# Optimization experiments

Measured on AMD Instinct MI355X. Metric: run time of the kernel, lower is better.

## Reference

```python
import jax, jax.numpy as jnp
import numpy as np
from jax import lax

K = 35
PAD = K // 2  # 17

def _maxpool_same(x):
    # x: [B, H, W]; torch MaxPool2d pads with -inf, stride 1, same spatial size
    return lax.reduce_window(
        x, -jnp.inf, lax.max,
        window_dimensions=(1, K, K),
        window_strides=(1, 1, 1),
        padding=[(0, 0), (PAD, PAD), (PAD, PAD)],
    )

def setup_inputs() -> dict:
    key = jax.random.key(0)
    k1, k2 = jax.random.split(key)
    shape = (16, 3, 512, 512)
    restored = jax.random.uniform(k1, shape, dtype=jnp.float32)
    target = jax.random.uniform(k2, shape, dtype=jnp.float32)
    return {"restored": restored, "target": target}

def reference(restored, target):
    r = _maxpool_same(jnp.min(restored, axis=1))  # channel-min then 35x35 max
    t = _maxpool_same(jnp.min(target, axis=1))
    out = jnp.mean(jnp.abs(r - t))
    return jax.nn.sigmoid(out)
```

## Files before the change

### kernel.cpp

```cpp
#include <hip/hip_runtime.h>
#include <math.h>

#define WID 512
#define HEI 512
#define NB  16
#define HW  ((size_t)HEI * WID)
#define NEG_INF (-INFINITY)

typedef float f4 __attribute__((ext_vector_type(4)));

__global__ __launch_bounds__(256) void hmax_kernel(
    const float* __restrict__ rin, const float* __restrict__ tin,
    float* __restrict__ ws, float* __restrict__ acc)
{
    __shared__ float sm[2][552];
    const int tid = threadIdx.x;
    const int row = tid >> 7;
    const int t   = tid & 127;
    const int h   = blockIdx.x * 2 + row;
    const int z   = blockIdx.y;
    const int b   = z & 15;
    const float* __restrict__ in = (z < NB) ? rin : tin;

    if (blockIdx.x == 0 && blockIdx.y == 0 && tid < 2) acc[tid] = 0.0f;

    if (tid < 80) {
        int r2 = tid / 40, j = tid % 40;
        sm[r2][(j < 20) ? j : (j + 512)] = NEG_INF;
    }

    const float* __restrict__ p = in + (size_t)b * 3 * HW + (size_t)h * WID;
    f4 a0 = __builtin_nontemporal_load((const f4*)p + t);
    f4 a1 = __builtin_nontemporal_load((const f4*)(p + HW) + t);
    f4 a2 = __builtin_nontemporal_load((const f4*)(p + 2 * HW) + t);
    f4 v;
    v.x = fminf(fminf(a0.x, a1.x), a2.x);
    v.y = fminf(fminf(a0.y, a1.y), a2.y);
    v.z = fminf(fminf(a0.z, a1.z), a2.z);
    v.w = fminf(fminf(a0.w, a1.w), a2.w);
    *(f4*)&sm[row][20 + 4 * t] = v;
    __syncthreads();

    const f4* __restrict__ smr = (const f4*)sm[row];
    f4 vv[11];
    #pragma unroll
    for (int i = 0; i < 11; ++i) vv[i] = smr[t + i];
    float q[10];
    #pragma unroll
    for (int i = 1; i <= 9; ++i)
        q[i] = fmaxf(fmaxf(vv[i].x, vv[i].y), fmaxf(vv[i].z, vv[i].w));
    float Q28 = fmaxf(fmaxf(fmaxf(q[2], q[3]), fmaxf(q[4], q[5])),
                      fmaxf(fmaxf(q[6], q[7]), q[8]));
    float Q18 = fmaxf(Q28, q[1]);
    float Q29 = fmaxf(Q28, q[9]);
    float s01 = fmaxf(vv[9].x, vv[9].y);
    float s23 = fmaxf(vv[1].z, vv[1].w);
    f4 o;
    o.x = fmaxf(fmaxf(Q18, vv[0].w), s01);
    o.y = fmaxf(Q18, fmaxf(s01, vv[9].z));
    o.z = fmaxf(fmaxf(Q29, vv[1].y), s23);
    o.w = fmaxf(Q29, fmaxf(s23, vv[10].x));
    *((f4*)(ws + (size_t)z * HW + (size_t)h * WID) + t) = o;
}

__global__ __launch_bounds__(256) void vmax_kernel(
    const float* __restrict__ ws, float* __restrict__ acc,
    float* __restrict__ out)
{
    __shared__ float sm[98][64];
    __shared__ float red[4];
    const int tid = threadIdx.x;
    const int col = tid & 63;
    const int ty  = tid >> 6;
    const int w0  = blockIdx.x * 64;
    const int h0  = blockIdx.y * 64;
    const int b   = blockIdx.z;

    float rtv[16];
    float tsum = 0.0f;

    #pragma unroll
    for (int tensor = 0; tensor < 2; ++tensor) {
        const float* __restrict__ pb = ws + (size_t)(tensor * NB + b) * HW;
        #pragma unroll
        for (int i0 = 0; i0 < 1568; i0 += 256) {
            int i = i0 + tid;
            if (i < 1568) {
                int r = i >> 4, c4 = i & 15;
                int hh = h0 - 17 + r;
                f4 v = {NEG_INF, NEG_INF, NEG_INF, NEG_INF};
                if (hh >= 0 && hh < HEI)
                    v = ((const f4*)pb)[hh * 128 + (w0 >> 2) + c4];
                *(f4*)&sm[r][c4 * 4] = v;
            }
        }
        __syncthreads();

        float vc[50];
        #pragma unroll
        for (int i = 0; i < 50; ++i) vc[i] = sm[ty * 16 + i][col];
        float q[12];
        #pragma unroll
        for (int i = 0; i < 12; ++i)
            q[i] = fmaxf(fmaxf(vc[4*i], vc[4*i+1]), fmaxf(vc[4*i+2], vc[4*i+3]));
        #pragma unroll
        for (int m = 0; m < 4; ++m) {
            float Qc = fmaxf(fmaxf(fmaxf(q[m+1], q[m+2]), fmaxf(q[m+3], q[m+4])),
                             fmaxf(fmaxf(q[m+5], q[m+6]), q[m+7]));
            float A  = fmaxf(Qc, q[m+8]);
            float o0 = fmaxf(fmaxf(Qc, q[m]),
                             fmaxf(fmaxf(vc[4*m+32], vc[4*m+33]), vc[4*m+34]));
            float o1 = fmaxf(A, fmaxf(fmaxf(vc[4*m+1], vc[4*m+2]), vc[4*m+3]));
            float o2 = fmaxf(A, fmaxf(fmaxf(vc[4*m+2], vc[4*m+3]), vc[4*m+36]));
            float o3 = fmaxf(A, fmaxf(fmaxf(vc[4*m+3], vc[4*m+36]), vc[4*m+37]));
            if (tensor == 0) {
                rtv[4*m] = o0; rtv[4*m+1] = o1; rtv[4*m+2] = o2; rtv[4*m+3] = o3;
            } else {
                tsum += fabsf(rtv[4*m]   - o0) + fabsf(rtv[4*m+1] - o1)
                      + fabsf(rtv[4*m+2] - o2) + fabsf(rtv[4*m+3] - o3);
            }
        }
        __syncthreads();
    }

    #pragma unroll
    for (int off = 32; off > 0; off >>= 1)
        tsum += __shfl_down(tsum, off, 64);
    if ((tid & 63) == 0) red[ty] = tsum;
    __syncthreads();
    if (tid == 0) {
        float blocksum = red[0] + red[1] + red[2] + red[3];
        atomicAdd(acc, blocksum);
        __threadfence();
        unsigned tk = atomicAdd((unsigned*)(acc + 1), 1u);
        if (tk == 1023u) {
            float s = atomicAdd(acc, 0.0f);
            out[0] = 1.0f / (1.0f + expf(-s / 4194304.0f));
        }
    }
}

extern "C" void kernel_launch(void* const* d_in, const int* in_sizes, int n_in,
                              void* d_out, int out_size, void* d_ws, size_t ws_size,
                              hipStream_t stream) {
    const float* rin = (const float*)d_in[0];
    const float* tin = (const float*)d_in[1];
    float* out = (float*)d_out;

    float* wsf = (float*)d_ws;
    float* acc = wsf + (size_t)2 * NB * HW;

    dim3 gA(HEI / 2, 2 * NB);
    hipLaunchKernelGGL(hmax_kernel, gA, dim3(256), 0, stream, rin, tin, wsf, acc);

    dim3 gB(WID / 64, HEI / 64, NB);
    hipLaunchKernelGGL(vmax_kernel, gB, dim3(256), 0, stream, wsf, acc, out);
}
```

Baseline: 154.0 us.

## Fuse channel-min, horizontal and vertical max pooling into one tiled kernel

Replaces the two-kernel pipeline with a single kernel. Each block loads a halo tile of the raw inputs, takes the channel minimum, runs the horizontal 35-wide max in shared memory, then the vertical max and the reduction. This removes the full-size intermediate write and read through global memory and one kernel launch. In exchange, each block recomputes channel-min and horizontal max over halo rows and columns (98x104 tile for a 64x64 output), re-reads overlapping input, and adds a memset launch to clear the accumulator.

```diff
diff --git a/kernel.cpp b/kernel.cpp
--- a/kernel.cpp
+++ b/kernel.cpp
@@ -9,46 +9,17 @@
 
 typedef float f4 __attribute__((ext_vector_type(4)));
 
-__global__ __launch_bounds__(256) void hmax_kernel(
-    const float* __restrict__ rin, const float* __restrict__ tin,
-    float* __restrict__ ws, float* __restrict__ acc)
-{
-    __shared__ float sm[2][552];
-    const int tid = threadIdx.x;
-    const int row = tid >> 7;
-    const int t   = tid & 127;
-    const int h   = blockIdx.x * 2 + row;
-    const int z   = blockIdx.y;
-    const int b   = z & 15;
-    const float* __restrict__ in = (z < NB) ? rin : tin;
+__device__ __forceinline__ float qmax4(f4 v) {
+    return fmaxf(fmaxf(v.x, v.y), fmaxf(v.z, v.w));
+}
 
-    if (blockIdx.x == 0 && blockIdx.y == 0 && tid < 2) acc[tid] = 0.0f;
-
-    if (tid < 80) {
-        int r2 = tid / 40, j = tid % 40;
-        sm[r2][(j < 20) ? j : (j + 512)] = NEG_INF;
-    }
-
-    const float* __restrict__ p = in + (size_t)b * 3 * HW + (size_t)h * WID;
-    f4 a0 = __builtin_nontemporal_load((const f4*)p + t);
-    f4 a1 = __builtin_nontemporal_load((const f4*)(p + HW) + t);
-    f4 a2 = __builtin_nontemporal_load((const f4*)(p + 2 * HW) + t);
-    f4 v;
-    v.x = fminf(fminf(a0.x, a1.x), a2.x);
-    v.y = fminf(fminf(a0.y, a1.y), a2.y);
-    v.z = fminf(fminf(a0.z, a1.z), a2.z);
-    v.w = fminf(fminf(a0.w, a1.w), a2.w);
-    *(f4*)&sm[row][20 + 4 * t] = v;
-    __syncthreads();
-
-    const f4* __restrict__ smr = (const f4*)sm[row];
+__device__ __forceinline__ f4 hwin35(const f4* __restrict__ rp, int c4) {
     f4 vv[11];
     #pragma unroll
-    for (int i = 0; i < 11; ++i) vv[i] = smr[t + i];
+    for (int i = 0; i < 11; ++i) vv[i] = rp[c4 + i];
     float q[10];
     #pragma unroll
-    for (int i = 1; i <= 9; ++i)
-        q[i] = fmaxf(fmaxf(vv[i].x, vv[i].y), fmaxf(vv[i].z, vv[i].w));
+    for (int i = 1; i <= 9; ++i) q[i] = qmax4(vv[i]);
     float Q28 = fmaxf(fmaxf(fmaxf(q[2], q[3]), fmaxf(q[4], q[5])),
                       fmaxf(fmaxf(q[6], q[7]), q[8]));
     float Q18 = fmaxf(Q28, q[1]);
@@ -60,45 +31,79 @@
     o.y = fmaxf(Q18, fmaxf(s01, vv[9].z));
     o.z = fmaxf(fmaxf(Q29, vv[1].y), s23);
     o.w = fmaxf(Q29, fmaxf(s23, vv[10].x));
-    *((f4*)(ws + (size_t)z * HW + (size_t)h * WID) + t) = o;
+    return o;
 }
 
-__global__ __launch_bounds__(256) void vmax_kernel(
-    const float* __restrict__ ws, float* __restrict__ acc,
-    float* __restrict__ out)
+__global__ __launch_bounds__(256, 3) void ccp_fused_kernel(
+    const float* __restrict__ rin, const float* __restrict__ tin,
+    float* __restrict__ acc, float* __restrict__ out)
 {
-    __shared__ float sm[98][64];
+    __shared__ float cm[98][104];
     __shared__ float red[4];
+
     const int tid = threadIdx.x;
     const int col = tid & 63;
     const int ty  = tid >> 6;
     const int w0  = blockIdx.x * 64;
     const int h0  = blockIdx.y * 64;
     const int b   = blockIdx.z;
+    const int gb  = (w0 - 20) >> 2;
 
     float rtv[16];
     float tsum = 0.0f;
 
     #pragma unroll
     for (int tensor = 0; tensor < 2; ++tensor) {
-        const float* __restrict__ pb = ws + (size_t)(tensor * NB + b) * HW;
+        const float* __restrict__ p =
+            ((tensor == 0) ? rin : tin) + (size_t)b * 3 * HW;
+
+        for (int i = tid; i < 3136; i += 256) {
+            int r = i >> 5, j = i & 31;
+            if (j < 26) {
+                int hh = h0 - 17 + r;
+                int gc = gb + j;
+                f4 v = {NEG_INF, NEG_INF, NEG_INF, NEG_INF};
+                if (hh >= 0 && hh < HEI && gc >= 0 && gc < (WID >> 2)) {
+                    const float* prow = p + (size_t)hh * WID;
+                    f4 a0 = ((const f4*)prow)[gc];
+                    f4 a1 = ((const f4*)(prow + HW))[gc];
+                    f4 a2 = ((const f4*)(prow + 2 * HW))[gc];
+                    v.x = fminf(fminf(a0.x, a1.x), a2.x);
+                    v.y = fminf(fminf(a0.y, a1.y), a2.y);
+                    v.z = fminf(fminf(a0.z, a1.z), a2.z);
+                    v.w = fminf(fminf(a0.w, a1.w), a2.w);
+                }
+                *(f4*)&cm[r][4 * j] = v;
+            }
+        }
+        __syncthreads();
+
+        f4 oA[4];
         #pragma unroll
-        for (int i0 = 0; i0 < 1568; i0 += 256) {
-            int i = i0 + tid;
-            if (i < 1568) {
-                int r = i >> 4, c4 = i & 15;
-                int hh = h0 - 17 + r;
-                f4 v = {NEG_INF, NEG_INF, NEG_INF, NEG_INF};
-                if (hh >= 0 && hh < HEI)
-                    v = ((const f4*)pb)[hh * 128 + (w0 >> 2) + c4];
-                *(f4*)&sm[r][c4 * 4] = v;
-            }
+        for (int k = 0; k < 4; ++k) {
+            int g = tid + (k << 8);
+            if (g < 784) oA[k] = hwin35((const f4*)&cm[g >> 4][0], g & 15);
+        }
+        __syncthreads();
+        f4 oB[4];
+        #pragma unroll
+        for (int k = 0; k < 4; ++k) {
+            int g = tid + (k << 8);
+            if (g < 784) *(f4*)&cm[g >> 4][4 * (g & 15)] = oA[k];
+            int g2 = g + 784;
+            if (g2 < 1568) oB[k] = hwin35((const f4*)&cm[g2 >> 4][0], g2 & 15);
+        }
+        __syncthreads();
+        #pragma unroll
+        for (int k = 0; k < 4; ++k) {
+            int g2 = tid + (k << 8) + 784;
+            if (g2 < 1568) *(f4*)&cm[g2 >> 4][4 * (g2 & 15)] = oB[k];
         }
         __syncthreads();
 
         float vc[50];
         #pragma unroll
-        for (int i = 0; i < 50; ++i) vc[i] = sm[ty * 16 + i][col];
+        for (int i = 0; i < 50; ++i) vc[i] = cm[ty * 16 + i][col];
         float q[12];
         #pragma unroll
         for (int i = 0; i < 12; ++i)
@@ -126,11 +131,11 @@
     #pragma unroll
     for (int off = 32; off > 0; off >>= 1)
         tsum += __shfl_down(tsum, off, 64);
-    if ((tid & 63) == 0) red[ty] = tsum;
+    if (col == 0) red[ty] = tsum;
     __syncthreads();
     if (tid == 0) {
-        float blocksum = red[0] + red[1] + red[2] + red[3];
-        atomicAdd(acc, blocksum);
+        float bs = red[0] + red[1] + red[2] + red[3];
+        atomicAdd(acc, bs);
         __threadfence();
         unsigned tk = atomicAdd((unsigned*)(acc + 1), 1u);
         if (tk == 1023u) {
@@ -146,13 +151,10 @@
     const float* rin = (const float*)d_in[0];
     const float* tin = (const float*)d_in[1];
     float* out = (float*)d_out;
+    float* acc = (float*)d_ws;
 
-    float* wsf = (float*)d_ws;
-    float* acc = wsf + (size_t)2 * NB * HW;
+    hipMemsetAsync(acc, 0, 2 * sizeof(float), stream);
 
-    dim3 gA(HEI / 2, 2 * NB);
-    hipLaunchKernelGGL(hmax_kernel, gA, dim3(256), 0, stream, rin, tin, wsf, acc);
-
-    dim3 gB(WID / 64, HEI / 64, NB);
-    hipLaunchKernelGGL(vmax_kernel, gB, dim3(256), 0, stream, wsf, acc, out);
+    dim3 g(WID / 64, HEI / 64, NB);
+    hipLaunchKernelGGL(ccp_fused_kernel, g, dim3(256), 0, stream, rin, tin, acc, out);
 }
```

New measurement: 164.7 us. +7.0%, slower.
